# Optimization experiments

Hardware: AMD Instinct MI355X
Metric: run time of the kernel (lower is better)

## Reference

```python
import jax, jax.numpy as jnp
import numpy as np

B, H, N = 256, 128, 1000

def setup_inputs() -> dict:
    key = jax.random.key(0)
    k1, k2, k3, k4, k5, k6 = jax.random.split(key, 6)
    return {
        "adj_hidden": jax.random.normal(k1, (B, H, N), dtype=jnp.float32),
        "static_hidden": jax.random.normal(k2, (B, H, N), dtype=jnp.float32),
        "dynamic_hidden": jax.random.normal(k3, (B, H, N), dtype=jnp.float32),
        "decoder_hidden": jax.random.normal(k4, (B, H), dtype=jnp.float32),
        "v": jax.random.normal(k5, (1, 1, H), dtype=jnp.float32) * 0.1,
        "W": jax.random.normal(k6, (1, H, 4 * H), dtype=jnp.float32) * 0.05,
    }

def reference(adj_hidden, static_hidden, dynamic_hidden, decoder_hidden, v, W):
    # hidden: [B, 4H, N] -- decoder_hidden broadcast along node dim
    dec = jnp.broadcast_to(decoder_hidden[:, :, None], static_hidden.shape)
    hidden = jnp.concatenate((adj_hidden, static_hidden, dynamic_hidden, dec), axis=1)
    # W[0]: [H, 4H]; scores: [B, H, N]
    Wh = jnp.tanh(jnp.einsum('hk,bkn->bhn', W[0], hidden))
    # v[0,0]: [H]; attns: [B, 1, N]
    attns = jnp.einsum('h,bhn->bn', v[0, 0], Wh)[:, None, :]
    return jax.nn.softmax(attns, axis=2)
```

## Files before the change

### kernel.cpp

```cpp
#include <hip/hip_runtime.h>
#include <hip/hip_fp16.h>
#include <cstdint>


#define BB 256
#define HH 128
#define NN 1000
#define K3 384
#define KH 192
#define WROW 400
#define WLDS (HH * WROW)
#define CT_OFF WLDS
#define VV_OFF (WLDS + 512)
#define SMEM_ATTN (WLDS + 1024)

typedef __attribute__((ext_vector_type(8))) _Float16 half8;
typedef __attribute__((ext_vector_type(4))) float f32x4;

__device__ __forceinline__ uint32_t pk_f16(float a, float b) {
    auto h = __builtin_amdgcn_cvt_pkrtz(a, b);
    return __builtin_bit_cast(uint32_t, h);
}
__device__ __forceinline__ float fast_tanh(float x) {
    float e = __expf(2.0f * x);
    return 1.0f - 2.0f * __builtin_amdgcn_rcpf(e + 1.0f);
}

__global__ void prep_kernel(const float* __restrict__ W, const float* __restrict__ dec,
                            uint16_t* __restrict__ Whf, float* __restrict__ cterm) {
    extern __shared__ float ls[];
    const int tid = threadIdx.x;
    if (blockIdx.x < 48) {
        int idx4 = blockIdx.x * 256 + tid;
        int h = idx4 / 96, k4 = idx4 - h * 96;
        float4 w = *(const float4*)(W + h * 512 + k4 * 4);
        union { __half hx[4]; uint2 u; } o;
        o.hx[0] = __float2half_rn(w.x);
        o.hx[1] = __float2half_rn(w.y);
        o.hx[2] = __float2half_rn(w.z);
        o.hx[3] = __float2half_rn(w.w);
        *(uint2*)(Whf + h * K3 + k4 * 4) = o.u;
    } else {
        float* w4 = ls;
        float* dl = ls + 128 * 129;
        const int bb = (blockIdx.x - 48) * 8;
#pragma unroll
        for (int i = 0; i < 16; ++i) {
            int chunk = tid + i * 256;
            int h = chunk >> 5, kq = chunk & 31;
            float4 v = *(const float4*)(W + h * 512 + 384 + kq * 4);
            float* d = w4 + h * 129 + kq * 4;
            d[0] = v.x; d[1] = v.y; d[2] = v.z; d[3] = v.w;
        }
        {
            float4 dv = *(const float4*)(dec + bb * HH + tid * 4);
            float* d = dl + tid * 4;
            d[0] = dv.x; d[1] = dv.y; d[2] = dv.z; d[3] = dv.w;
        }
        __syncthreads();
#pragma unroll
        for (int r = 0; r < 4; ++r) {
            int o = tid + r * 256;
            int h = o & 127, bl_ = o >> 7;
            const float* wr = w4 + h * 129;
            const float* dr = dl + bl_ * 128;
            float s = 0.f;
#pragma unroll 8
            for (int k = 0; k < 128; ++k) s += wr[k] * dr[k];
            cterm[(bb + bl_) * HH + h] = s;
        }
    }
}

__launch_bounds__(512, 6)
__global__ void attn_main(const float* __restrict__ adj, const float* __restrict__ sta,
                          const float* __restrict__ dyn,
                          const uint16_t* __restrict__ Whf,
                          const float* __restrict__ cterm, const float* __restrict__ vvec,
                          float* __restrict__ logits) {
    extern __shared__ char smem[];
    const int tid = threadIdx.x;
    const int b = blockIdx.x >> 3;
    const int tile = blockIdx.x & 7;

    const int wave = tid >> 6, lane = tid & 63;
    const int c = lane & 15, q = lane >> 4;
    const int n = tile * 128 + wave * 16 + c;
    const int ncl = (n < NN) ? n : NN - 1;
    const long bbase = (long)b * HH * NN;
    const float* A0 = adj + bbase;
    const float* A1 = sta + bbase;
    const float* A2 = dyn + bbase;

    f32x4 acc[8];
#pragma unroll
    for (int m = 0; m < 8; ++m) acc[m] = (f32x4){0.f, 0.f, 0.f, 0.f};

    union bu { uint32_t u[4]; half8 h; };
    bu bcur;

    {
        const float* px = A0 + (8 * q) * NN + ncl;
        float x0[8];
#pragma unroll
        for (int j = 0; j < 8; ++j) x0[j] = px[j * NN];
#pragma unroll
        for (int j = 0; j < 4; ++j) bcur.u[j] = pk_f16(x0[2 * j], x0[2 * j + 1]);
    }

#pragma unroll
    for (int pp = 0; pp < 2; ++pp) {
        if (pp) __syncthreads();
#pragma unroll
        for (int i = 0; i < 6; ++i) {
            int ch = tid + i * 512;
            int hr = ch / 24, j = ch - hr * 24;
            *(uint4*)(smem + hr * WROW + j * 16) =
                *(const uint4*)(Whf + hr * K3 + pp * KH + j * 8);
        }
        if (pp == 0) {
            if (tid < 32) {
                ((float4*)(smem + CT_OFF))[tid] = ((const float4*)(cterm + b * HH))[tid];
            } else if (tid < 64) {
                ((float4*)(smem + VV_OFF))[tid - 32] = ((const float4*)vvec)[tid - 32];
            }
        }
        __syncthreads();

#pragma unroll
        for (int it = 0; it < 6; ++it) {
            const int kk = pp * 6 + it;
            float xf[8];
            if (kk + 1 < 12) {
                const int t2 = (kk + 1) >> 2, cc2 = (kk + 1) & 3;
                const float* base2 = (t2 == 0) ? A0 : ((t2 == 1) ? A1 : A2);
                const float* px = base2 + (cc2 * 32 + 8 * q) * NN + ncl;
#pragma unroll
                for (int j = 0; j < 8; ++j) xf[j] = px[j * NN];
            }
            const int rowoff = it * 64 + q * 16;
#pragma unroll
            for (int m = 0; m < 8; ++m) {
                const half8 av = *(const half8*)(smem + (m * 16 + c) * WROW + rowoff);
                acc[m] = __builtin_amdgcn_mfma_f32_16x16x32_f16(av, bcur.h, acc[m], 0, 0, 0);
            }
            if (kk + 1 < 12) {
#pragma unroll
                for (int j = 0; j < 4; ++j) bcur.u[j] = pk_f16(xf[2 * j], xf[2 * j + 1]);
            }
        }
    }

    const float* ct = (const float*)(smem + CT_OFF);
    const float* vv = (const float*)(smem + VV_OFF);
    float s = 0.0f;
#pragma unroll
    for (int m = 0; m < 8; ++m) {
#pragma unroll
        for (int r = 0; r < 4; ++r) {
            const int h = m * 16 + q * 4 + r;
            s += vv[h] * fast_tanh(acc[m][r] + ct[h]);
        }
    }
    s += __shfl_xor(s, 16, 64);
    s += __shfl_xor(s, 32, 64);
    if (lane < 16 && n < NN) logits[b * NN + n] = s;
}

__global__ void softmax_kernel(float* __restrict__ out) {
    const int b = blockIdx.x;
    const int tid = threadIdx.x;
    float* row = out + b * NN;

    float vals[4];
#pragma unroll
    for (int i = 0; i < 4; ++i) {
        int j = tid + i * 256;
        vals[i] = (j < NN) ? row[j] : -1e30f;
    }
    float mx = fmaxf(fmaxf(vals[0], vals[1]), fmaxf(vals[2], vals[3]));
#pragma unroll
    for (int off = 1; off < 64; off <<= 1) mx = fmaxf(mx, __shfl_xor(mx, off, 64));
    __shared__ float smax[4];
    if ((tid & 63) == 0) smax[tid >> 6] = mx;
    __syncthreads();
    mx = fmaxf(fmaxf(smax[0], smax[1]), fmaxf(smax[2], smax[3]));

    float e[4];
    float s = 0.0f;
#pragma unroll
    for (int i = 0; i < 4; ++i) {
        int j = tid + i * 256;
        e[i] = (j < NN) ? __expf(vals[i] - mx) : 0.0f;
        s += e[i];
    }
#pragma unroll
    for (int off = 1; off < 64; off <<= 1) s += __shfl_xor(s, off, 64);
    __shared__ float ssum[4];
    if ((tid & 63) == 0) ssum[tid >> 6] = s;
    __syncthreads();
    s = ssum[0] + ssum[1] + ssum[2] + ssum[3];
    float inv = 1.0f / s;
#pragma unroll
    for (int i = 0; i < 4; ++i) {
        int j = tid + i * 256;
        if (j < NN) row[j] = e[i] * inv;
    }
}

extern "C" void kernel_launch(void* const* d_in, const int* in_sizes, int n_in,
                              void* d_out, int out_size, void* d_ws, size_t ws_size,
                              hipStream_t stream) {
    const float* adj = (const float*)d_in[0];
    const float* sta = (const float*)d_in[1];
    const float* dyn = (const float*)d_in[2];
    const float* dec = (const float*)d_in[3];
    const float* v   = (const float*)d_in[4];
    const float* W   = (const float*)d_in[5];

    uint16_t* Whf = (uint16_t*)d_ws;
    float* cterm  = (float*)(Whf + HH * K3);
    float* logits = (float*)d_out;

    prep_kernel<<<80, 256, (128 * 129 + 1024) * 4, stream>>>(W, dec, Whf, cterm);
    attn_main<<<BB * 8, 512, SMEM_ATTN, stream>>>(adj, sta, dyn, Whf, cterm, v, logits);
    softmax_kernel<<<BB, 256, 0, stream>>>(logits);
}
```

Baseline: 360.1 us.

## Stage activation tiles through double-buffered LDS with vectorized coalesced loads

Each thread now loads activations as two float4 vectors from contiguous columns, converts them to fp16, and writes them into a double-buffered LDS tile. This replaces the old pattern of eight strided scalar loads per lane, which fetched only narrow 64-byte segments. Loads are issued two K-steps ahead, and the second half of W is fetched into registers mid-loop to overlap with compute. The cost is a barrier on every K step, more LDS per block, and a lower occupancy hint (4 instead of 6).

```diff
diff --git a/kernel.cpp b/kernel.cpp
--- a/kernel.cpp
+++ b/kernel.cpp
@@ -12,7 +12,9 @@
 #define WLDS (HH * WROW)
 #define CT_OFF WLDS
 #define VV_OFF (WLDS + 512)
-#define SMEM_ATTN (WLDS + 1024)
+#define XB0 (WLDS + 1024)
+#define XB1 (XB0 + 8192)
+#define SMEM_ATTN (XB1 + 8192)
 
 typedef __attribute__((ext_vector_type(8))) _Float16 half8;
 typedef __attribute__((ext_vector_type(4))) float f32x4;
@@ -72,7 +74,7 @@
     }
 }
 
-__launch_bounds__(512, 6)
+__launch_bounds__(512, 4)
 __global__ void attn_main(const float* __restrict__ adj, const float* __restrict__ sta,
                           const float* __restrict__ dyn,
                           const uint16_t* __restrict__ Whf,
@@ -86,70 +88,101 @@
     const int wave = tid >> 6, lane = tid & 63;
     const int c = lane & 15, q = lane >> 4;
     const int n = tile * 128 + wave * 16 + c;
-    const int ncl = (n < NN) ? n : NN - 1;
+    const int nl = wave * 16 + c;
     const long bbase = (long)b * HH * NN;
     const float* A0 = adj + bbase;
     const float* A1 = sta + bbase;
     const float* A2 = dyn + bbase;
 
+    const int kp = tid >> 5, n4 = tid & 31;
+    int colg = tile * 128 + n4 * 4;
+    if (colg > 996) colg = 996;
+
     f32x4 acc[8];
 #pragma unroll
     for (int m = 0; m < 8; ++m) acc[m] = (f32x4){0.f, 0.f, 0.f, 0.f};
 
+    float4 sa0, sb0, sa1, sb1;
+    uint4 wreg[6];
+
+#define XISSUE(T, RA, RB)                                                          \
+    {                                                                              \
+        const int t2_ = (T) >> 2, cc_ = (T) & 3;                                   \
+        const float* base2_ = (t2_ == 0) ? A0 : ((t2_ == 1) ? A1 : A2);            \
+        const float* p_ = base2_ + (cc_ * 32 + 2 * kp) * NN + colg;                \
+        RA = *(const float4*)p_;                                                   \
+        RB = *(const float4*)(p_ + NN);                                            \
+    }
+#define XWRITE(T, RA, RB)                                                          \
+    {                                                                              \
+        uint4 o_;                                                                  \
+        o_.x = pk_f16(RA.x, RB.x); o_.y = pk_f16(RA.y, RB.y);                      \
+        o_.z = pk_f16(RA.z, RB.z); o_.w = pk_f16(RA.w, RB.w);                      \
+        *(uint4*)(smem + (((T) & 1) ? XB1 : XB0) + kp * 512 + n4 * 16) = o_;       \
+    }
+
+    XISSUE(0, sa0, sb0);
+    XISSUE(1, sa1, sb1);
+#pragma unroll
+    for (int i = 0; i < 6; ++i) {
+        int ch = tid + i * 512;
+        int hr = ch / 24, j = ch - hr * 24;
+        *(uint4*)(smem + hr * WROW + j * 16) = *(const uint4*)(Whf + hr * K3 + j * 8);
+    }
+    if (tid < 32) {
+        ((float4*)(smem + CT_OFF))[tid] = ((const float4*)(cterm + b * HH))[tid];
+    } else if (tid < 64) {
+        ((float4*)(smem + VV_OFF))[tid - 32] = ((const float4*)vvec)[tid - 32];
+    }
+    XWRITE(0, sa0, sb0);
+    __syncthreads();
+
     union bu { uint32_t u[4]; half8 h; };
-    bu bcur;
-
-    {
-        const float* px = A0 + (8 * q) * NN + ncl;
-        float x0[8];
-#pragma unroll
-        for (int j = 0; j < 8; ++j) x0[j] = px[j * NN];
-#pragma unroll
-        for (int j = 0; j < 4; ++j) bcur.u[j] = pk_f16(x0[2 * j], x0[2 * j + 1]);
-    }
-
-#pragma unroll
-    for (int pp = 0; pp < 2; ++pp) {
-        if (pp) __syncthreads();
-#pragma unroll
-        for (int i = 0; i < 6; ++i) {
-            int ch = tid + i * 512;
-            int hr = ch / 24, j = ch - hr * 24;
-            *(uint4*)(smem + hr * WROW + j * 16) =
-                *(const uint4*)(Whf + hr * K3 + pp * KH + j * 8);
-        }
-        if (pp == 0) {
-            if (tid < 32) {
-                ((float4*)(smem + CT_OFF))[tid] = ((const float4*)(cterm + b * HH))[tid];
-            } else if (tid < 64) {
-                ((float4*)(smem + VV_OFF))[tid - 32] = ((const float4*)vvec)[tid - 32];
+
+#pragma unroll
+    for (int t = 0; t < 12; ++t) {
+        if (t + 2 < 12) {
+            if ((t & 1) == 0) { XISSUE(t + 2, sa0, sb0); }
+            else              { XISSUE(t + 2, sa1, sb1); }
+        }
+        if (t == 4) {
+#pragma unroll
+            for (int i = 0; i < 6; ++i) {
+                int ch = tid + i * 512;
+                int hr = ch / 24, j = ch - hr * 24;
+                wreg[i] = *(const uint4*)(Whf + hr * K3 + KH + j * 8);
             }
         }
-        __syncthreads();
-
-#pragma unroll
-        for (int it = 0; it < 6; ++it) {
-            const int kk = pp * 6 + it;
-            float xf[8];
-            if (kk + 1 < 12) {
-                const int t2 = (kk + 1) >> 2, cc2 = (kk + 1) & 3;
-                const float* base2 = (t2 == 0) ? A0 : ((t2 == 1) ? A1 : A2);
-                const float* px = base2 + (cc2 * 32 + 8 * q) * NN + ncl;
-#pragma unroll
-                for (int j = 0; j < 8; ++j) xf[j] = px[j * NN];
+        if (t == 6) {
+#pragma unroll
+            for (int i = 0; i < 6; ++i) {
+                int ch = tid + i * 512;
+                int hr = ch / 24, j = ch - hr * 24;
+                *(uint4*)(smem + hr * WROW + j * 16) = wreg[i];
             }
-            const int rowoff = it * 64 + q * 16;
-#pragma unroll
-            for (int m = 0; m < 8; ++m) {
-                const half8 av = *(const half8*)(smem + (m * 16 + c) * WROW + rowoff);
-                acc[m] = __builtin_amdgcn_mfma_f32_16x16x32_f16(av, bcur.h, acc[m], 0, 0, 0);
-            }
-            if (kk + 1 < 12) {
-#pragma unroll
-                for (int j = 0; j < 4; ++j) bcur.u[j] = pk_f16(xf[2 * j], xf[2 * j + 1]);
-            }
-        }
-    }
+            __syncthreads();
+        }
+
+        bu bf;
+        const uint32_t* xb = (const uint32_t*)(smem + ((t & 1) ? XB1 : XB0));
+#pragma unroll
+        for (int jj = 0; jj < 4; ++jj) bf.u[jj] = xb[(q * 4 + jj) * 128 + nl];
+        const int it6 = (t >= 6) ? (t - 6) : t;
+        const int rowoff = it6 * 64 + q * 16;
+#pragma unroll
+        for (int m = 0; m < 8; ++m) {
+            const half8 av = *(const half8*)(smem + (m * 16 + c) * WROW + rowoff);
+            acc[m] = __builtin_amdgcn_mfma_f32_16x16x32_f16(av, bf.h, acc[m], 0, 0, 0);
+        }
+
+        if (t + 1 < 12) {
+            if ((t & 1) == 0) { XWRITE(t + 1, sa1, sb1); }
+            else              { XWRITE(t + 1, sa0, sb0); }
+        }
+        if (t < 11) __syncthreads();
+    }
+#undef XISSUE
+#undef XWRITE
 
     const float* ct = (const float*)(smem + CT_OFF);
     const float* vv = (const float*)(smem + VV_OFF);
```

Result: slower. 381.4 us (+5.9%).
